# Optimization experiments

Measured on AMD Instinct MI355X. Metric: run time of the kernel, lower is better.

The kernel has to match this reference:

```python
import jax, jax.numpy as jnp
import numpy as np

NUM_KEYPOINTS = 2048
SAMPLE_RADIUS = 1.6
NUM_SECTORS = 6
NEG = jnp.float32(-1e10)
POS = jnp.float32(1e10)


def setup_inputs() -> dict:
    key = jax.random.key(0)
    kxy, kz, kc, kcz, kd, ky = jax.random.split(key, 6)
    B, N, M = 2, 65536, 128
    pts_xy = jax.random.uniform(kxy, (B, N, 2), minval=-70.0, maxval=70.0)
    pts_z = jax.random.uniform(kz, (B, N, 1), minval=-3.0, maxval=1.0)
    points = jnp.concatenate([pts_xy, pts_z], axis=-1)  # [B,N,3]
    ctr_xy = jax.random.uniform(kc, (B, M, 2), minval=-60.0, maxval=60.0)
    ctr_z = jax.random.uniform(kcz, (B, M, 1), minval=-2.0, maxval=0.0)
    dims = jax.random.uniform(kd, (B, M, 3), minval=1.0, maxval=4.5)
    yaw = jax.random.uniform(ky, (B, M, 1), minval=-np.pi, maxval=np.pi)
    rois = jnp.concatenate([ctr_xy, ctr_z, dims, yaw], axis=-1)  # [B,M,7]
    return {"points": points, "rois": rois}


def _masked_fps(xyz, mask, K):
    """Farthest point sampling restricted to mask; returns K indices into xyz.
    Matches mmcv furthest_point_sample: squared distances, start at first point."""
    first = jnp.argmax(mask)  # first valid point in original order
    dmin = jnp.where(mask, POS, NEG)

    def step(carry, _):
        dmin, last = carry
        d = jnp.sum((xyz - xyz[last]) ** 2, axis=-1)
        dmin = jnp.minimum(dmin, jnp.where(mask, d, NEG))
        nxt = jnp.argmax(dmin)
        return (dmin, nxt), nxt

    (_, _), rest = jax.lax.scan(step, (dmin, first), None, length=K - 1)
    return jnp.concatenate([first[None], rest])  # [K]


def _spc_single(points, rois):
    """points: [N,3] float, rois: [M,7]. Returns [NUM_KEYPOINTS,3]."""
    N = points.shape[0]
    K = NUM_KEYPOINTS
    # geometric center: z += dz/2 (done in forward before sampling)
    rois = rois.at[:, 2].add(rois[:, 5] * 0.5)
    # --- sample_points_with_roi: point-to-ROI-center distance filter ---
    diff = points[:, None, :] - rois[None, :, 0:3]          # [N,M,3]
    dist = jnp.linalg.norm(diff, axis=-1)                   # [N,M]
    min_dis = jnp.min(dist, axis=-1)
    min_idx = jnp.argmin(dist, axis=-1)
    roi_max_dim = jnp.linalg.norm(rois[min_idx, 3:6] * 0.5, axis=-1)
    valid = min_dis < roi_max_dim + SAMPLE_RADIUS           # [N]
    total = jnp.maximum(jnp.sum(valid), 1)
    # --- sector_fps ---
    sector_size = 2.0 * np.pi / NUM_SECTORS
    angles = jnp.arctan2(points[:, 1], points[:, 0]) + np.pi
    sector = jnp.clip(jnp.floor(angles / sector_size), 0, NUM_SECTORS).astype(jnp.int32)
    masks = valid[None, :] & (sector[None, :] == jnp.arange(NUM_SECTORS)[:, None])  # [S,N]
    cnt = jnp.sum(masks, axis=-1)                           # [S]
    # per-sector budget: min(cnt_k, ceil(cnt_k / total * K)), 0 for empty sectors
    n_k = jnp.minimum(cnt, jnp.ceil(cnt.astype(jnp.float32) * K / total).astype(cnt.dtype))
    fps_idx = jax.vmap(_masked_fps, in_axes=(None, 0, None))(points, masks, K)  # [S,K]
    # concatenate the first n_k picks of each sector in sector order
    offsets = jnp.concatenate([jnp.zeros((1,), n_k.dtype), jnp.cumsum(n_k)[:-1]])
    pos = offsets[:, None] + jnp.arange(K)[None, :]          # [S,K] slot in concat order
    keep = jnp.arange(K)[None, :] < n_k[:, None]
    pos = jnp.where(keep, pos, K)                            # out-of-range -> dropped
    buf = jnp.zeros((K,), jnp.int32)
    buf = buf.at[pos.reshape(-1)].set(fps_idx.reshape(-1).astype(jnp.int32), mode='drop')
    # truncate / cyclic-repeat to exactly K keypoints
    s_total = jnp.maximum(jnp.sum(n_k), 1)
    out_idx = buf[jnp.arange(K) % s_total]
    return points[out_idx]                                   # [K,3]


def reference(points, rois):
    return jax.vmap(_spc_single)(points, rois)  # [B,K,3]
```

## Files before the change

### kernel.cpp

```cpp
#include <hip/hip_runtime.h>
#include <cmath>
#include <cstdint>

#pragma clang fp contract(off)

#define B_ 2
#define N_ 65536
#define M_ 128
#define K_ 2048
#define S_ 6
#define NBLK 256
#define CT 256
#define FPS_T 512
#define NW 8
#define RMAX 8
#define CAP (FPS_T * RMAX)

#define PI_F 3.14159265358979323846f
#define SS_F 1.0471975511965976f

__device__ __forceinline__ unsigned long long wave_max_u64_dpp(unsigned long long key) {
#define DPP_STEP(CTRL)                                                          \
    {                                                                           \
        unsigned lo = (unsigned)key, hi = (unsigned)(key >> 32);                \
        unsigned olo = (unsigned)__builtin_amdgcn_update_dpp(0, (int)lo, CTRL, 0xf, 0xf, true); \
        unsigned ohi = (unsigned)__builtin_amdgcn_update_dpp(0, (int)hi, CTRL, 0xf, 0xf, true); \
        unsigned long long o = ((unsigned long long)ohi << 32) | olo;           \
        if (o > key) key = o;                                                   \
    }
    DPP_STEP(0x111)
    DPP_STEP(0x112)
    DPP_STEP(0x114)
    DPP_STEP(0x118)
    DPP_STEP(0x142)
    DPP_STEP(0x143)
#undef DPP_STEP
    return key;
}

__global__ __launch_bounds__(CT)
void k_classify(const float* __restrict__ points, const float* __restrict__ rois,
                int* __restrict__ sec_id, int* __restrict__ blkcnt) {
    __shared__ float4 sroi[M_];
    __shared__ int lc[8];
    int blk = blockIdx.x;
    int gid = blk * CT + threadIdx.x;
    int b = gid >> 16;
    if (threadIdx.x < M_) {
        const float* r = rois + ((size_t)b * M_ + threadIdx.x) * 7;
        float cz = r[2] + r[5] * 0.5f;
        float hx = r[3] * 0.5f, hy = r[4] * 0.5f, hz = r[5] * 0.5f;
        sroi[threadIdx.x] = make_float4(r[0], r[1], cz, sqrtf((hx*hx + hy*hy) + hz*hz));
    }
    if (threadIdx.x < 8) lc[threadIdx.x] = 0;
    __syncthreads();

    const float* p = points + (size_t)gid * 3;
    float px = p[0], py = p[1], pz = p[2];
    float best = 1e30f; int bi = 0;
    for (int m = 0; m < M_; m++) {
        float4 c = sroi[m];
        float dx = px - c.x, dy = py - c.y, dz = pz - c.z;
        float d = sqrtf((dx*dx + dy*dy) + dz*dz);
        if (d < best) { best = d; bi = m; }
    }
    bool valid = best < (sroi[bi].w + 1.6f);

    float a = atan2f(py, px) + PI_F;
    float fs = floorf(a / SS_F);
    fs = fminf(fmaxf(fs, 0.0f), 6.0f);
    int sec = (int)fs;

    sec_id[gid] = valid ? sec : -1;
    if (valid) atomicAdd(&lc[sec], 1);
    __syncthreads();
    if (threadIdx.x < 8) blkcnt[blk * 8 + threadIdx.x] = lc[threadIdx.x];
}

__global__ void k_plan(const int* __restrict__ blkcnt, int* __restrict__ bbase,
                       int* __restrict__ cnt, int* __restrict__ offv,
                       int* __restrict__ n_needed, int* __restrict__ sec_base,
                       int* __restrict__ s_total) {
    __shared__ int scnt[2][8];
    int t = threadIdx.x;
    if (t < 16) scnt[t >> 3][t & 7] = 0;
    __syncthreads();
    if (t < 14) {
        int b = t / 7, s = t % 7;
        int run = 0;
        #pragma unroll 16
        for (int j = 0; j < NBLK; j++) {
            int blk = b * NBLK + j;
            int c = blkcnt[blk * 8 + s];
            if (s < 6) bbase[blk * 6 + s] = run;
            run += c;
        }
        scnt[b][s] = run;
        cnt[b * 8 + s] = run;
    }
    __syncthreads();
    if (t < B_) {
        int b = t;
        int total = 0;
        for (int s = 0; s < 7; s++) total += scnt[b][s];
        if (total < 1) total = 1;
        int sb = 0, snk = 0;
        for (int s = 0; s < 6; s++) {
            int cs = scnt[b][s];
            int nk = (int)ceilf((float)cs * 2048.0f / (float)total);
            if (nk > cs) nk = cs;
            offv[b * 6 + s] = snk;
            int need = 0;
            if (snk < K_) { need = K_ - snk; if (need > nk) need = nk; }
            n_needed[b * 6 + s] = need;
            sec_base[b * 6 + s] = sb;
            sb += cs; snk += nk;
        }
        s_total[b] = (snk < 1) ? 1 : snk;
    }
}

__global__ __launch_bounds__(CT)
void k_compact(const float* __restrict__ points, const int* __restrict__ sec_id,
               const int* __restrict__ sec_base, const int* __restrict__ bbase,
               int* __restrict__ comp_idx, float4* __restrict__ comp_xyz) {
    __shared__ int lc[4 * 6];
    __shared__ int sbase[6], blkb[6];
    int blk = blockIdx.x;
    int b = blk >> 8;
    int tid = threadIdx.x, lane = tid & 63, wid = tid >> 6;
    if (tid < 6) sbase[tid] = sec_base[b * 6 + tid];
    else if (tid >= 64 && tid < 70) blkb[tid - 64] = bbase[blk * 6 + (tid - 64)];
    int gid = blk * CT + tid;
    int sec = sec_id[gid];
    unsigned long long mymask = 0;
    for (int s = 0; s < 6; s++) {
        unsigned long long m = __ballot(sec == s);
        if (sec == s) mymask = m;
        if (lane == 0) lc[wid * 6 + s] = __popcll(m);
    }
    __syncthreads();
    if (sec >= 0 && sec < 6) {
        int woff = 0;
        for (int w = 0; w < wid; w++) woff += lc[w * 6 + sec];
        int rank = __popcll(mymask & ((1ull << lane) - 1ull));
        int addr = b * N_ + sbase[sec] + blkb[sec] + woff + rank;
        const float* p = points + (size_t)gid * 3;
        comp_idx[addr] = gid & (N_ - 1);
        comp_xyz[addr] = make_float4(p[0], p[1], p[2], 0.0f);
    }
}

__global__ __launch_bounds__(FPS_T, 2)
void k_fps(const int* __restrict__ cnt, const int* __restrict__ sec_base,
           const int* __restrict__ offv, const int* __restrict__ n_needed,
           const float4* __restrict__ comp_xyz,
           float* __restrict__ dmin_g, int* __restrict__ buf) {
    __shared__ float4 sxyz[CAP];
    __shared__ int pick_lds[K_];
    __shared__ unsigned long long skey[2][NW];
    int b = blockIdx.x / S_, s = blockIdx.x % S_;
    int need = n_needed[b * 6 + s];
    if (need <= 0) return;
    int cs = cnt[b * 8 + s];
    int base = b * N_ + sec_base[b * 6 + s];
    const float4* cxyz = comp_xyz + base;
    int off = b * K_ + offv[b * 6 + s];
    int tid = threadIdx.x, lane = tid & 63, wid = tid >> 6;

    if (cs <= CAP) {
        float px[RMAX], py[RMAX], pz[RMAX], dmv[RMAX];
        #pragma unroll
        for (int r = 0; r < RMAX; r++) {
            if (r * FPS_T < cs) {
                int i = tid + r * FPS_T;
                if (i < cs) {
                    float4 q = cxyz[i];
                    sxyz[i] = q;
                    px[r] = q.x; py[r] = q.y; pz[r] = q.z;
                    dmv[r] = 1e10f;
                }
            }
        }
        if (tid == 0) pick_lds[0] = 0;
        __syncthreads();
        float4 l4 = sxyz[0];
        float lx = l4.x, ly = l4.y, lz = l4.z;

        #pragma unroll 1
        for (int k = 1; k < need; k++) {
            unsigned long long t[4] = {0ull, 0ull, 0ull, 0ull};
            #pragma unroll
            for (int r = 0; r < RMAX; r++) {
                if (r * FPS_T < cs) {
                    int i = tid + r * FPS_T;
                    if (i < cs) {
                        float dx = px[r] - lx, dy = py[r] - ly, dz = pz[r] - lz;
                        float d = (dx*dx + dy*dy) + dz*dz;
                        float nd = fminf(dmv[r], d);
                        dmv[r] = nd;
                        unsigned long long kk =
                            ((unsigned long long)__float_as_uint(nd) << 32) | (unsigned)(~(unsigned)i);
                        if (kk > t[r & 3]) t[r & 3] = kk;
                    }
                }
            }
            unsigned long long ta = (t[1] > t[0]) ? t[1] : t[0];
            unsigned long long tb = (t[3] > t[2]) ? t[3] : t[2];
            unsigned long long key = (tb > ta) ? tb : ta;
            key = wave_max_u64_dpp(key);
            int par = k & 1;
            if (lane == 63) skey[par][wid] = key;
            __syncthreads();
            unsigned long long q0 = skey[par][0], q1 = skey[par][1];
            unsigned long long q2 = skey[par][2], q3 = skey[par][3];
            unsigned long long q4 = skey[par][4], q5 = skey[par][5];
            unsigned long long q6 = skey[par][6], q7 = skey[par][7];
            q0 = (q1 > q0) ? q1 : q0;
            q2 = (q3 > q2) ? q3 : q2;
            q4 = (q5 > q4) ? q5 : q4;
            q6 = (q7 > q6) ? q7 : q6;
            q0 = (q2 > q0) ? q2 : q0;
            q4 = (q6 > q4) ? q6 : q4;
            unsigned long long bk = (q4 > q0) ? q4 : q0;
            int bix = (int)(~(unsigned)(bk & 0xFFFFFFFFull));
            if (tid == 0) pick_lds[k] = bix;
            float4 n4 = sxyz[bix];
            lx = n4.x; ly = n4.y; lz = n4.z;
        }
        __syncthreads();
        #pragma unroll 1
        for (int i = tid; i < need; i += FPS_T)
            buf[off + i] = base + pick_lds[i];
    } else {
        float* dm = dmin_g + base;
        if (tid == 0) pick_lds[0] = 0;
        __syncthreads();
        float4 f0 = cxyz[0];
        float lx = f0.x, ly = f0.y, lz = f0.z;
        #pragma unroll 1
        for (int k = 1; k < need; k++) {
            unsigned long long key = 0;
            #pragma unroll 1
            for (int i = tid; i < cs; i += FPS_T) {
                float4 q = cxyz[i];
                float dx = q.x - lx, dy = q.y - ly, dz = q.z - lz;
                float d = (dx*dx + dy*dy) + dz*dz;
                float prev = (k == 1) ? 1e10f : dm[i];
                float nd = fminf(prev, d);
                dm[i] = nd;
                unsigned long long kk =
                    ((unsigned long long)__float_as_uint(nd) << 32) | (unsigned)(~(unsigned)i);
                if (kk > key) key = kk;
            }
            key = wave_max_u64_dpp(key);
            int par = k & 1;
            if (lane == 63) skey[par][wid] = key;
            __syncthreads();
            unsigned long long q0 = skey[par][0], q1 = skey[par][1];
            unsigned long long q2 = skey[par][2], q3 = skey[par][3];
            unsigned long long q4 = skey[par][4], q5 = skey[par][5];
            unsigned long long q6 = skey[par][6], q7 = skey[par][7];
            q0 = (q1 > q0) ? q1 : q0;
            q2 = (q3 > q2) ? q3 : q2;
            q4 = (q5 > q4) ? q5 : q4;
            q6 = (q7 > q6) ? q7 : q6;
            q0 = (q2 > q0) ? q2 : q0;
            q4 = (q6 > q4) ? q6 : q4;
            unsigned long long bk = (q4 > q0) ? q4 : q0;
            int bix = (int)(~(unsigned)(bk & 0xFFFFFFFFull));
            if (tid == 0) pick_lds[k] = bix;
            float4 n4 = cxyz[bix];
            lx = n4.x; ly = n4.y; lz = n4.z;
        }
        __syncthreads();
        #pragma unroll 1
        for (int i = tid; i < need; i += FPS_T)
            buf[off + i] = base + pick_lds[i];
    }
}

__global__ void k_out(const float* __restrict__ points, const int* __restrict__ buf,
                      const int* __restrict__ comp_idx, const int* __restrict__ s_total,
                      float* __restrict__ out) {
    int i = blockIdx.x * 256 + threadIdx.x;
    if (i >= B_ * K_) return;
    int b = i / K_, j = i % K_;
    int st = s_total[b];
    int g = buf[b * K_ + (j % st)];
    int idx = comp_idx[g];
    const float* p = points + ((size_t)b * N_ + idx) * 3;
    float* o = out + (size_t)i * 3;
    o[0] = p[0]; o[1] = p[1]; o[2] = p[2];
}

extern "C" void kernel_launch(void* const* d_in, const int* in_sizes, int n_in,
                              void* d_out, int out_size, void* d_ws, size_t ws_size,
                              hipStream_t stream) {
    const float* points = (const float*)d_in[0];
    const float* rois   = (const float*)d_in[1];
    float* out = (float*)d_out;

    char* w = (char*)d_ws;
    auto carve = [&](size_t bytes) -> char* {
        char* p = w; w += (bytes + 255) & ~(size_t)255; return p;
    };
    int*    sec_id   = (int*)   carve((size_t)B_ * N_ * sizeof(int));
    int*    blkcnt   = (int*)   carve((size_t)B_ * NBLK * 8 * sizeof(int));
    int*    bbase    = (int*)   carve((size_t)B_ * NBLK * 6 * sizeof(int));
    int*    cnt      = (int*)   carve((size_t)B_ * 8 * sizeof(int));
    int*    offv     = (int*)   carve((size_t)B_ * 6 * sizeof(int));
    int*    n_needed = (int*)   carve((size_t)B_ * 6 * sizeof(int));
    int*    sec_base = (int*)   carve((size_t)B_ * 6 * sizeof(int));
    int*    s_total  = (int*)   carve((size_t)B_ * sizeof(int));
    int*    buf      = (int*)   carve((size_t)B_ * K_ * sizeof(int));
    int*    comp_idx = (int*)   carve((size_t)B_ * N_ * sizeof(int));
    float4* comp_xyz = (float4*)carve((size_t)B_ * N_ * sizeof(float4));
    float*  dmin_g   = (float*) carve((size_t)B_ * N_ * sizeof(float));

    hipLaunchKernelGGL(k_classify, dim3(B_ * NBLK), dim3(CT), 0, stream,
                       points, rois, sec_id, blkcnt);
    hipLaunchKernelGGL(k_plan, dim3(1), dim3(64), 0, stream,
                       blkcnt, bbase, cnt, offv, n_needed, sec_base, s_total);
    hipLaunchKernelGGL(k_compact, dim3(B_ * NBLK), dim3(CT), 0, stream,
                       points, sec_id, sec_base, bbase, comp_idx, comp_xyz);
    hipLaunchKernelGGL(k_fps, dim3(B_ * S_), dim3(FPS_T), 0, stream,
                       cnt, sec_base, offv, n_needed, comp_xyz, dmin_g, buf);
    hipLaunchKernelGGL(k_out, dim3((B_ * K_ + 255) / 256), dim3(256), 0, stream,
                       points, buf, comp_idx, s_total, out);
}
```

Before: 436.2 us.

## Pack two FPS sector chains into one 1024-thread block

The FPS kernel now runs two independent sector chains (batch 0 and batch 1 of the same sector) in one 1024-thread block. The halves share a __syncthreads per iteration but keep separate LDS arrays and reductions. The grid drops from 12 blocks to 6, and shared memory per block doubles to roughly 128KB. The two chains now move in lockstep up to the larger pick count, and each barrier spans 16 waves, which may add sync cost to a latency-bound serial loop.

Result: slower. 721.6 us (+65.5%).

```diff
diff --git a/kernel.cpp b/kernel.cpp
--- a/kernel.cpp
+++ b/kernel.cpp
@@ -12,6 +12,7 @@
 #define NBLK 256
 #define CT 256
 #define FPS_T 512
+#define PAIR_T 1024
 #define NW 8
 #define RMAX 8
 #define CAP (FPS_T * RMAX)
@@ -151,71 +152,109 @@
     }
 }
 
-__global__ __launch_bounds__(FPS_T, 2)
+__global__ __launch_bounds__(PAIR_T)
 void k_fps(const int* __restrict__ cnt, const int* __restrict__ sec_base,
            const int* __restrict__ offv, const int* __restrict__ n_needed,
            const float4* __restrict__ comp_xyz,
            float* __restrict__ dmin_g, int* __restrict__ buf) {
-    __shared__ float4 sxyz[CAP];
-    __shared__ int pick_lds[K_];
-    __shared__ unsigned long long skey[2][NW];
-    int b = blockIdx.x / S_, s = blockIdx.x % S_;
-    int need = n_needed[b * 6 + s];
-    if (need <= 0) return;
+    __shared__ float4 sxyz[2][CAP];
+    __shared__ int pick_lds[2][K_];
+    __shared__ unsigned long long skey[2][2][NW];
+    int tid = threadIdx.x;
+    int half = tid >> 9;
+    int ltid = tid & (FPS_T - 1);
+    int lane = tid & 63;
+    int w8 = (tid >> 6) & 7;
+
+    int c0 = blockIdx.x, c1 = blockIdx.x + S_;
+    int n0 = n_needed[(c0 / S_) * 6 + (c0 % S_)];
+    int n1 = n_needed[(c1 / S_) * 6 + (c1 % S_)];
+    int kmax = n0 > n1 ? n0 : n1;
+    if (kmax <= 0) return;
+
+    int chain = half ? c1 : c0;
+    int b = chain / S_, s = chain % S_;
+    int need = half ? n1 : n0;
     int cs = cnt[b * 8 + s];
     int base = b * N_ + sec_base[b * 6 + s];
     const float4* cxyz = comp_xyz + base;
     int off = b * K_ + offv[b * 6 + s];
-    int tid = threadIdx.x, lane = tid & 63, wid = tid >> 6;
-
-    if (cs <= CAP) {
-        float px[RMAX], py[RMAX], pz[RMAX], dmv[RMAX];
+    float* dm = dmin_g + base;
+    bool fast = (cs <= CAP);
+
+    float px[RMAX], py[RMAX], pz[RMAX], dmv[RMAX];
+    if (fast && need > 0) {
         #pragma unroll
         for (int r = 0; r < RMAX; r++) {
             if (r * FPS_T < cs) {
-                int i = tid + r * FPS_T;
+                int i = ltid + r * FPS_T;
                 if (i < cs) {
                     float4 q = cxyz[i];
-                    sxyz[i] = q;
+                    sxyz[half][i] = q;
                     px[r] = q.x; py[r] = q.y; pz[r] = q.z;
                     dmv[r] = 1e10f;
                 }
             }
         }
-        if (tid == 0) pick_lds[0] = 0;
-        __syncthreads();
-        float4 l4 = sxyz[0];
-        float lx = l4.x, ly = l4.y, lz = l4.z;
-
-        #pragma unroll 1
-        for (int k = 1; k < need; k++) {
-            unsigned long long t[4] = {0ull, 0ull, 0ull, 0ull};
-            #pragma unroll
-            for (int r = 0; r < RMAX; r++) {
-                if (r * FPS_T < cs) {
-                    int i = tid + r * FPS_T;
-                    if (i < cs) {
-                        float dx = px[r] - lx, dy = py[r] - ly, dz = pz[r] - lz;
-                        float d = (dx*dx + dy*dy) + dz*dz;
-                        float nd = fminf(dmv[r], d);
-                        dmv[r] = nd;
-                        unsigned long long kk =
-                            ((unsigned long long)__float_as_uint(nd) << 32) | (unsigned)(~(unsigned)i);
-                        if (kk > t[r & 3]) t[r & 3] = kk;
+    }
+    if (ltid == 0) pick_lds[half][0] = 0;
+    __syncthreads();
+    float lx = 0.0f, ly = 0.0f, lz = 0.0f;
+    if (need > 0) {
+        if (fast) { float4 l4 = sxyz[half][0]; lx = l4.x; ly = l4.y; lz = l4.z; }
+        else      { float4 l4 = cxyz[0];       lx = l4.x; ly = l4.y; lz = l4.z; }
+    }
+
+    #pragma unroll 1
+    for (int k = 1; k < kmax; k++) {
+        unsigned long long key = 0;
+        if (k < need) {
+            if (fast) {
+                unsigned long long t[4] = {0ull, 0ull, 0ull, 0ull};
+                #pragma unroll
+                for (int r = 0; r < RMAX; r++) {
+                    if (r * FPS_T < cs) {
+                        int i = ltid + r * FPS_T;
+                        if (i < cs) {
+                            float dx = px[r] - lx, dy = py[r] - ly, dz = pz[r] - lz;
+                            float d = (dx*dx + dy*dy) + dz*dz;
+                            float nd = fminf(dmv[r], d);
+                            dmv[r] = nd;
+                            unsigned long long kk =
+                                ((unsigned long long)__float_as_uint(nd) << 32)
+                                | (unsigned)(~(unsigned)i);
+                            if (kk > t[r & 3]) t[r & 3] = kk;
+                        }
                     }
                 }
+                unsigned long long ta = (t[1] > t[0]) ? t[1] : t[0];
+                unsigned long long tb = (t[3] > t[2]) ? t[3] : t[2];
+                key = (tb > ta) ? tb : ta;
+            } else {
+                #pragma unroll 1
+                for (int i = ltid; i < cs; i += FPS_T) {
+                    float4 q = cxyz[i];
+                    float dx = q.x - lx, dy = q.y - ly, dz = q.z - lz;
+                    float d = (dx*dx + dy*dy) + dz*dz;
+                    float prev = (k == 1) ? 1e10f : dm[i];
+                    float nd = fminf(prev, d);
+                    dm[i] = nd;
+                    unsigned long long kk =
+                        ((unsigned long long)__float_as_uint(nd) << 32)
+                        | (unsigned)(~(unsigned)i);
+                    if (kk > key) key = kk;
+                }
             }
-            unsigned long long ta = (t[1] > t[0]) ? t[1] : t[0];
-            unsigned long long tb = (t[3] > t[2]) ? t[3] : t[2];
-            unsigned long long key = (tb > ta) ? tb : ta;
-            key = wave_max_u64_dpp(key);
-            int par = k & 1;
-            if (lane == 63) skey[par][wid] = key;
-            __syncthreads();
-            unsigned long long q0 = skey[par][0], q1 = skey[par][1];
-            unsigned long long q2 = skey[par][2], q3 = skey[par][3];
-            unsigned long long q4 = skey[par][4], q5 = skey[par][5];
-            unsigned long long q6 = skey[par][6], q7 = skey[par][7];
+        }
+        key = wave_max_u64_dpp(key);
+        int par = k & 1;
+        if (lane == 63) skey[half][par][w8] = key;
+        __syncthreads();
+        if (k < need) {
+            unsigned long long q0 = skey[half][par][0], q1 = skey[half][par][1];
+            unsigned long long q2 = skey[half][par][2], q3 = skey[half][par][3];
+            unsigned long long q4 = skey[half][par][4], q5 = skey[half][par][5];
+            unsigned long long q6 = skey[half][par][6], q7 = skey[half][par][7];
             q0 = (q1 > q0) ? q1 : q0;
             q2 = (q3 > q2) ? q3 : q2;
             q4 = (q5 > q4) ? q5 : q4;
@@ -224,59 +263,21 @@
             q4 = (q6 > q4) ? q6 : q4;
             unsigned long long bk = (q4 > q0) ? q4 : q0;
             int bix = (int)(~(unsigned)(bk & 0xFFFFFFFFull));
-            if (tid == 0) pick_lds[k] = bix;
-            float4 n4 = sxyz[bix];
-            lx = n4.x; ly = n4.y; lz = n4.z;
-        }
-        __syncthreads();
+            if (ltid == 0) pick_lds[half][k] = bix;
+            if (fast) {
+                float4 n4 = sxyz[half][bix];
+                lx = n4.x; ly = n4.y; lz = n4.z;
+            } else {
+                float4 n4 = cxyz[bix];
+                lx = n4.x; ly = n4.y; lz = n4.z;
+            }
+        }
+    }
+    __syncthreads();
+    if (need > 0) {
         #pragma unroll 1
-        for (int i = tid; i < need; i += FPS_T)
-            buf[off + i] = base + pick_lds[i];
-    } else {
-        float* dm = dmin_g + base;
-        if (tid == 0) pick_lds[0] = 0;
-        __syncthreads();
-        float4 f0 = cxyz[0];
-        float lx = f0.x, ly = f0.y, lz = f0.z;
-        #pragma unroll 1
-        for (int k = 1; k < need; k++) {
-            unsigned long long key = 0;
-            #pragma unroll 1
-            for (int i = tid; i < cs; i += FPS_T) {
-                float4 q = cxyz[i];
-                float dx = q.x - lx, dy = q.y - ly, dz = q.z - lz;
-                float d = (dx*dx + dy*dy) + dz*dz;
-                float prev = (k == 1) ? 1e10f : dm[i];
-                float nd = fminf(prev, d);
-                dm[i] = nd;
-                unsigned long long kk =
-                    ((unsigned long long)__float_as_uint(nd) << 32) | (unsigned)(~(unsigned)i);
-                if (kk > key) key = kk;
-            }
-            key = wave_max_u64_dpp(key);
-            int par = k & 1;
-            if (lane == 63) skey[par][wid] = key;
-            __syncthreads();
-            unsigned long long q0 = skey[par][0], q1 = skey[par][1];
-            unsigned long long q2 = skey[par][2], q3 = skey[par][3];
-            unsigned long long q4 = skey[par][4], q5 = skey[par][5];
-            unsigned long long q6 = skey[par][6], q7 = skey[par][7];
-            q0 = (q1 > q0) ? q1 : q0;
-            q2 = (q3 > q2) ? q3 : q2;
-            q4 = (q5 > q4) ? q5 : q4;
-            q6 = (q7 > q6) ? q7 : q6;
-            q0 = (q2 > q0) ? q2 : q0;
-            q4 = (q6 > q4) ? q6 : q4;
-            unsigned long long bk = (q4 > q0) ? q4 : q0;
-            int bix = (int)(~(unsigned)(bk & 0xFFFFFFFFull));
-            if (tid == 0) pick_lds[k] = bix;
-            float4 n4 = cxyz[bix];
-            lx = n4.x; ly = n4.y; lz = n4.z;
-        }
-        __syncthreads();
-        #pragma unroll 1
-        for (int i = tid; i < need; i += FPS_T)
-            buf[off + i] = base + pick_lds[i];
+        for (int i = ltid; i < need; i += FPS_T)
+            buf[off + i] = base + pick_lds[half][i];
     }
 }
 
@@ -324,7 +325,7 @@
                        blkcnt, bbase, cnt, offv, n_needed, sec_base, s_total);
     hipLaunchKernelGGL(k_compact, dim3(B_ * NBLK), dim3(CT), 0, stream,
                        points, sec_id, sec_base, bbase, comp_idx, comp_xyz);
-    hipLaunchKernelGGL(k_fps, dim3(B_ * S_), dim3(FPS_T), 0, stream,
+    hipLaunchKernelGGL(k_fps, dim3((B_ * S_) / 2), dim3(PAIR_T), 0, stream,
                        cnt, sec_base, offv, n_needed, comp_xyz, dmin_g, buf);
     hipLaunchKernelGGL(k_out, dim3((B_ * K_ + 255) / 256), dim3(256), 0, stream,
                        points, buf, comp_idx, s_total, out);
```

## Fold plan kernel into compact and output gather into FPS last block

Applied to the files above, without the earlier changes.

Removes the single-block planning kernel by having every compact block redundantly load all block counts into LDS and compute its own prefix and sector bases, with block 0 of each batch writing the global plan arrays. The output gather kernel is merged into the FPS kernel using an atomic done-counter so the last finishing block performs the gather. The FPS inner loop drops the per-element bounds check by zero-initialising padded slots. This saves two kernel launches and their gaps in exchange for redundant per-block scans and a serial tail gather in one block.

Result: slower. 487.6 us (+11.8%).

```diff
diff --git a/kernel.cpp b/kernel.cpp
--- a/kernel.cpp
+++ b/kernel.cpp
@@ -40,12 +40,14 @@
 
 __global__ __launch_bounds__(CT)
 void k_classify(const float* __restrict__ points, const float* __restrict__ rois,
-                int* __restrict__ sec_id, int* __restrict__ blkcnt) {
+                int* __restrict__ sec_id, int* __restrict__ blkcnt,
+                int* __restrict__ done_ctr) {
     __shared__ float4 sroi[M_];
     __shared__ int lc[8];
     int blk = blockIdx.x;
     int gid = blk * CT + threadIdx.x;
     int b = gid >> 16;
+    if (blk == 0 && threadIdx.x == 0) *done_ctr = 0;
     if (threadIdx.x < M_) {
         const float* r = rois + ((size_t)b * M_ + threadIdx.x) * 7;
         float cz = r[2] + r[5] * 0.5f;
@@ -77,60 +79,61 @@
     if (threadIdx.x < 8) blkcnt[blk * 8 + threadIdx.x] = lc[threadIdx.x];
 }
 
-__global__ void k_plan(const int* __restrict__ blkcnt, int* __restrict__ bbase,
-                       int* __restrict__ cnt, int* __restrict__ offv,
-                       int* __restrict__ n_needed, int* __restrict__ sec_base,
-                       int* __restrict__ s_total) {
-    __shared__ int scnt[2][8];
-    int t = threadIdx.x;
-    if (t < 16) scnt[t >> 3][t & 7] = 0;
-    __syncthreads();
-    if (t < 14) {
-        int b = t / 7, s = t % 7;
-        int run = 0;
-        #pragma unroll 16
-        for (int j = 0; j < NBLK; j++) {
-            int blk = b * NBLK + j;
-            int c = blkcnt[blk * 8 + s];
-            if (s < 6) bbase[blk * 6 + s] = run;
-            run += c;
-        }
-        scnt[b][s] = run;
-        cnt[b * 8 + s] = run;
-    }
-    __syncthreads();
-    if (t < B_) {
-        int b = t;
+__global__ __launch_bounds__(CT)
+void k_compact(const float* __restrict__ points, const int* __restrict__ sec_id,
+               const int* __restrict__ blkcnt,
+               int* __restrict__ cnt, int* __restrict__ offv,
+               int* __restrict__ n_needed, int* __restrict__ sec_base_g,
+               int* __restrict__ s_total,
+               int* __restrict__ comp_idx, float4* __restrict__ comp_xyz) {
+    __shared__ int scnt_lds[NBLK][8];
+    __shared__ int sbase[6], blkb[6], stot[8];
+    __shared__ int lc[4 * 6];
+    int blk = blockIdx.x;
+    int b = blk >> 8, j = blk & 255;
+    int tid = threadIdx.x, lane = tid & 63, wid = tid >> 6;
+
+    {
+        const int4* src = (const int4*)(blkcnt + (size_t)(b * NBLK + tid) * 8);
+        int4 r0 = src[0], r1 = src[1];
+        *(int4*)&scnt_lds[tid][0] = r0;
+        *(int4*)&scnt_lds[tid][4] = r1;
+    }
+    __syncthreads();
+    if (tid < 7) {
+        int run = 0, pref = 0;
+        for (int j2 = 0; j2 < NBLK; j2++) {
+            if (j2 == j) pref = run;
+            run += scnt_lds[j2][tid];
+        }
+        stot[tid] = run;
+        if (tid < 6) blkb[tid] = pref;
+    }
+    __syncthreads();
+    if (tid == 0) {
+        int sb = 0;
+        for (int s = 0; s < 6; s++) { sbase[s] = sb; sb += stot[s]; }
+    }
+    if (j == 0 && tid == 64) {
         int total = 0;
-        for (int s = 0; s < 7; s++) total += scnt[b][s];
+        for (int s = 0; s < 7; s++) total += stot[s];
         if (total < 1) total = 1;
         int sb = 0, snk = 0;
         for (int s = 0; s < 6; s++) {
-            int cs = scnt[b][s];
+            int cs = stot[s];
             int nk = (int)ceilf((float)cs * 2048.0f / (float)total);
             if (nk > cs) nk = cs;
             offv[b * 6 + s] = snk;
             int need = 0;
             if (snk < K_) { need = K_ - snk; if (need > nk) need = nk; }
             n_needed[b * 6 + s] = need;
-            sec_base[b * 6 + s] = sb;
+            sec_base_g[b * 6 + s] = sb;
+            cnt[b * 8 + s] = cs;
             sb += cs; snk += nk;
         }
         s_total[b] = (snk < 1) ? 1 : snk;
     }
-}
-
-__global__ __launch_bounds__(CT)
-void k_compact(const float* __restrict__ points, const int* __restrict__ sec_id,
-               const int* __restrict__ sec_base, const int* __restrict__ bbase,
-               int* __restrict__ comp_idx, float4* __restrict__ comp_xyz) {
-    __shared__ int lc[4 * 6];
-    __shared__ int sbase[6], blkb[6];
-    int blk = blockIdx.x;
-    int b = blk >> 8;
-    int tid = threadIdx.x, lane = tid & 63, wid = tid >> 6;
-    if (tid < 6) sbase[tid] = sec_base[b * 6 + tid];
-    else if (tid >= 64 && tid < 70) blkb[tid - 64] = bbase[blk * 6 + (tid - 64)];
+
     int gid = blk * CT + tid;
     int sec = sec_id[gid];
     unsigned long long mymask = 0;
@@ -155,32 +158,31 @@
 void k_fps(const int* __restrict__ cnt, const int* __restrict__ sec_base,
            const int* __restrict__ offv, const int* __restrict__ n_needed,
            const float4* __restrict__ comp_xyz,
-           float* __restrict__ dmin_g, int* __restrict__ buf) {
+           float* __restrict__ dmin_g, int* __restrict__ buf,
+           const float* __restrict__ points, const int* __restrict__ comp_idx,
+           const int* __restrict__ s_total, float* __restrict__ out,
+           int* __restrict__ done_ctr) {
     __shared__ float4 sxyz[CAP];
     __shared__ int pick_lds[K_];
     __shared__ unsigned long long skey[2][NW];
+    __shared__ int is_last;
     int b = blockIdx.x / S_, s = blockIdx.x % S_;
     int need = n_needed[b * 6 + s];
-    if (need <= 0) return;
     int cs = cnt[b * 8 + s];
     int base = b * N_ + sec_base[b * 6 + s];
     const float4* cxyz = comp_xyz + base;
     int off = b * K_ + offv[b * 6 + s];
     int tid = threadIdx.x, lane = tid & 63, wid = tid >> 6;
 
-    if (cs <= CAP) {
+    if (need > 0 && cs <= CAP) {
         float px[RMAX], py[RMAX], pz[RMAX], dmv[RMAX];
         #pragma unroll
         for (int r = 0; r < RMAX; r++) {
-            if (r * FPS_T < cs) {
-                int i = tid + r * FPS_T;
-                if (i < cs) {
-                    float4 q = cxyz[i];
-                    sxyz[i] = q;
-                    px[r] = q.x; py[r] = q.y; pz[r] = q.z;
-                    dmv[r] = 1e10f;
-                }
-            }
+            int i = tid + r * FPS_T;
+            float4 q = make_float4(0.0f, 0.0f, 0.0f, 0.0f);
+            float d0 = 0.0f;
+            if (i < cs) { q = cxyz[i]; sxyz[i] = q; d0 = 1e10f; }
+            px[r] = q.x; py[r] = q.y; pz[r] = q.z; dmv[r] = d0;
         }
         if (tid == 0) pick_lds[0] = 0;
         __syncthreads();
@@ -194,15 +196,14 @@
             for (int r = 0; r < RMAX; r++) {
                 if (r * FPS_T < cs) {
                     int i = tid + r * FPS_T;
-                    if (i < cs) {
-                        float dx = px[r] - lx, dy = py[r] - ly, dz = pz[r] - lz;
-                        float d = (dx*dx + dy*dy) + dz*dz;
-                        float nd = fminf(dmv[r], d);
-                        dmv[r] = nd;
-                        unsigned long long kk =
-                            ((unsigned long long)__float_as_uint(nd) << 32) | (unsigned)(~(unsigned)i);
-                        if (kk > t[r & 3]) t[r & 3] = kk;
-                    }
+                    float dx = px[r] - lx, dy = py[r] - ly, dz = pz[r] - lz;
+                    float d = (dx*dx + dy*dy) + dz*dz;
+                    float nd = fminf(dmv[r], d);
+                    dmv[r] = nd;
+                    unsigned long long kk =
+                        ((unsigned long long)__float_as_uint(nd) << 32)
+                        | (unsigned)(~(unsigned)i);
+                    if (kk > t[r & 3]) t[r & 3] = kk;
                 }
             }
             unsigned long long ta = (t[1] > t[0]) ? t[1] : t[0];
@@ -232,7 +233,7 @@
         #pragma unroll 1
         for (int i = tid; i < need; i += FPS_T)
             buf[off + i] = base + pick_lds[i];
-    } else {
+    } else if (need > 0) {
         float* dm = dmin_g + base;
         if (tid == 0) pick_lds[0] = 0;
         __syncthreads();
@@ -278,20 +279,27 @@
         for (int i = tid; i < need; i += FPS_T)
             buf[off + i] = base + pick_lds[i];
     }
-}
-
-__global__ void k_out(const float* __restrict__ points, const int* __restrict__ buf,
-                      const int* __restrict__ comp_idx, const int* __restrict__ s_total,
-                      float* __restrict__ out) {
-    int i = blockIdx.x * 256 + threadIdx.x;
-    if (i >= B_ * K_) return;
-    int b = i / K_, j = i % K_;
-    int st = s_total[b];
-    int g = buf[b * K_ + (j % st)];
-    int idx = comp_idx[g];
-    const float* p = points + ((size_t)b * N_ + idx) * 3;
-    float* o = out + (size_t)i * 3;
-    o[0] = p[0]; o[1] = p[1]; o[2] = p[2];
+
+    __syncthreads();
+    if (tid == 0) {
+        __threadfence();
+        int old = atomicAdd(done_ctr, 1);
+        is_last = (old == B_ * S_ - 1) ? 1 : 0;
+    }
+    __syncthreads();
+    if (is_last) {
+        __threadfence();
+        #pragma unroll 1
+        for (int i = tid; i < B_ * K_; i += FPS_T) {
+            int b2 = i / K_, j2 = i - b2 * K_;
+            int st = s_total[b2];
+            int g = buf[b2 * K_ + (j2 % st)];
+            int idx = comp_idx[g];
+            const float* p = points + ((size_t)b2 * N_ + idx) * 3;
+            float* o = out + (size_t)i * 3;
+            o[0] = p[0]; o[1] = p[1]; o[2] = p[2];
+        }
+    }
 }
 
 extern "C" void kernel_launch(void* const* d_in, const int* in_sizes, int n_in,
@@ -307,7 +315,6 @@
     };
     int*    sec_id   = (int*)   carve((size_t)B_ * N_ * sizeof(int));
     int*    blkcnt   = (int*)   carve((size_t)B_ * NBLK * 8 * sizeof(int));
-    int*    bbase    = (int*)   carve((size_t)B_ * NBLK * 6 * sizeof(int));
     int*    cnt      = (int*)   carve((size_t)B_ * 8 * sizeof(int));
     int*    offv     = (int*)   carve((size_t)B_ * 6 * sizeof(int));
     int*    n_needed = (int*)   carve((size_t)B_ * 6 * sizeof(int));
@@ -317,15 +324,14 @@
     int*    comp_idx = (int*)   carve((size_t)B_ * N_ * sizeof(int));
     float4* comp_xyz = (float4*)carve((size_t)B_ * N_ * sizeof(float4));
     float*  dmin_g   = (float*) carve((size_t)B_ * N_ * sizeof(float));
+    int*    done_ctr = (int*)   carve(sizeof(int));
 
     hipLaunchKernelGGL(k_classify, dim3(B_ * NBLK), dim3(CT), 0, stream,
-                       points, rois, sec_id, blkcnt);
-    hipLaunchKernelGGL(k_plan, dim3(1), dim3(64), 0, stream,
-                       blkcnt, bbase, cnt, offv, n_needed, sec_base, s_total);
+                       points, rois, sec_id, blkcnt, done_ctr);
     hipLaunchKernelGGL(k_compact, dim3(B_ * NBLK), dim3(CT), 0, stream,
-                       points, sec_id, sec_base, bbase, comp_idx, comp_xyz);
+                       points, sec_id, blkcnt, cnt, offv, n_needed, sec_base,
+                       s_total, comp_idx, comp_xyz);
     hipLaunchKernelGGL(k_fps, dim3(B_ * S_), dim3(FPS_T), 0, stream,
-                       cnt, sec_base, offv, n_needed, comp_xyz, dmin_g, buf);
-    hipLaunchKernelGGL(k_out, dim3((B_ * K_ + 255) / 256), dim3(256), 0, stream,
-                       points, buf, comp_idx, s_total, out);
-}
+                       cnt, sec_base, offv, n_needed, comp_xyz, dmin_g, buf,
+                       points, comp_idx, s_total, out, done_ctr);
+}
```
